# Optimization experiments

Measured on AMD Instinct MI355X. Metric: run time of the kernel, lower is better.

The kernel has to match this reference:

```python
import jax, jax.numpy as jnp
import numpy as np

H = 4096
N_HEADS = 32
N_KV = 8
HEAD_DIM = H // N_HEADS  # 128
GROUPS = N_HEADS // N_KV  # 4
FFN = 11008
EPS = 1e-5
B = 16
S_CACHE = 4096


def _rms(x, w):
    var = jnp.mean(x * x, axis=-1, keepdims=True)
    return w * (x * jax.lax.rsqrt(var + EPS))


def setup_inputs() -> dict:
    key = jax.random.key(0)
    ks = jax.random.split(key, 12)
    s = 0.02
    return {
        "hidden_states": jax.random.normal(ks[0], (B, 1, H), jnp.float32),
        "k_cache": jax.random.normal(ks[1], (B, N_KV, S_CACHE, HEAD_DIM), jnp.float32),
        "v_cache": jax.random.normal(ks[2], (B, N_KV, S_CACHE, HEAD_DIM), jnp.float32),
        "Wq": jax.random.normal(ks[3], (N_HEADS * HEAD_DIM, H), jnp.float32) * s,
        "Wk": jax.random.normal(ks[4], (N_KV * HEAD_DIM, H), jnp.float32) * s,
        "Wv": jax.random.normal(ks[5], (N_KV * HEAD_DIM, H), jnp.float32) * s,
        "Wo": jax.random.normal(ks[6], (H, N_HEADS * HEAD_DIM), jnp.float32) * s,
        "Wg": jax.random.normal(ks[7], (FFN, H), jnp.float32) * s,
        "Wu": jax.random.normal(ks[8], (FFN, H), jnp.float32) * s,
        "Wd": jax.random.normal(ks[9], (H, FFN), jnp.float32) * s,
        "ln1_w": jnp.ones((H,), jnp.float32),
        "ln2_w": jnp.ones((H,), jnp.float32),
    }


def reference(hidden_states, k_cache, v_cache, Wq, Wk, Wv, Wo, Wg, Wu, Wd, ln1_w, ln2_w):
    b = hidden_states.shape[0]
    residual = hidden_states
    h = _rms(hidden_states, ln1_w)  # [B,1,H]

    q = (h @ Wq.T).reshape(b, N_KV, GROUPS, HEAD_DIM)       # [B,kvH,G,D]
    k_new = (h @ Wk.T).reshape(b, N_KV, 1, HEAD_DIM)         # [B,kvH,1,D]
    v_new = (h @ Wv.T).reshape(b, N_KV, 1, HEAD_DIM)

    k = jnp.concatenate([k_cache, k_new], axis=2)            # [B,kvH,S+1,D]
    v = jnp.concatenate([v_cache, v_new], axis=2)

    scale = 1.0 / np.sqrt(HEAD_DIM)
    # GQA without materializing repeated KV heads (same math as repeat_interleave)
    scores = jnp.einsum("bkgd,bksd->bkgs", q, k) * scale      # [B,kvH,G,S+1]
    probs = jax.nn.softmax(scores.astype(jnp.float32), axis=-1).astype(q.dtype)
    attn = jnp.einsum("bkgs,bksd->bkgd", probs, v)            # [B,kvH,G,D]
    attn = attn.reshape(b, 1, N_HEADS * HEAD_DIM)

    h = residual + attn @ Wo.T                                # [B,1,H]

    residual = h
    h = _rms(h, ln2_w)
    mlp = (jax.nn.silu(h @ Wg.T) * (h @ Wu.T)) @ Wd.T
    return residual + mlp
```

## Files before the change

### kernel.cpp

```cpp
#include <hip/hip_runtime.h>
#include <math.h>

#define HH   4096
#define NKV  8
#define GRP  4
#define HD   128
#define FFN  11008
#define NB   16
#define SC   4096
#define SCALE 0.08838834764831845f
#define SCH  512

typedef float f4v __attribute__((ext_vector_type(4)));
typedef float f32x4 __attribute__((ext_vector_type(4)));
typedef short bf16x8 __attribute__((ext_vector_type(8)));
typedef unsigned short u16x4 __attribute__((ext_vector_type(4)));

__device__ __forceinline__ f4v ntload4(const float* p) {
  return __builtin_nontemporal_load((const f4v*)p);
}
__device__ __forceinline__ float dot4(f4v a, f4v b) {
  return a[0] * b[0] + a[1] * b[1] + a[2] * b[2] + a[3] * b[3];
}
__device__ __forceinline__ unsigned short f2bf(float f) {
  unsigned int u = __builtin_bit_cast(unsigned int, f);
  u += 0x7fffu + ((u >> 16) & 1u);
  return (unsigned short)(u >> 16);
}

__global__ void rmsnorm_bf_k(const float* __restrict__ x, const float* __restrict__ w,
                             unsigned short* __restrict__ y) {
  int b = blockIdx.x;
  const float* xb = x + (size_t)b * HH;
  unsigned short* yb = y + (size_t)b * HH;
  int t = threadIdx.x, lane = t & 63, wave = t >> 6;
  f4v v[4];
  float ss = 0.f;
#pragma unroll
  for (int i = 0; i < 4; ++i) {
    v[i] = *(const f4v*)(xb + 4 * (t + 256 * i));
    ss += dot4(v[i], v[i]);
  }
#pragma unroll
  for (int m = 1; m < 64; m <<= 1) ss += __shfl_xor(ss, m);
  __shared__ float red[4];
  if (lane == 0) red[wave] = ss;
  __syncthreads();
  float tot = red[0] + red[1] + red[2] + red[3];
  float rs = rsqrtf(tot * (1.0f / HH) + 1e-5f);
#pragma unroll
  for (int i = 0; i < 4; ++i) {
    int h = 4 * (t + 256 * i);
    f4v wv = *(const f4v*)(w + h);
    f4v o = v[i] * rs * wv;
    u16x4 p;
#pragma unroll
    for (int j = 0; j < 4; ++j) p[j] = f2bf(o[j]);
    *(u16x4*)(yb + h) = p;
  }
}

template <int MODE>
__global__ __launch_bounds__(256, 4) void gemv_mfma_k(
    const float* __restrict__ W0, const float* __restrict__ W1,
    const float* __restrict__ W2, const unsigned short* __restrict__ xbf,
    float* __restrict__ part, int O, int H, int CH) {
  int t = threadIdx.x, lane = t & 63, wave = t >> 6;
  int rb = blockIdx.x, kc = blockIdx.y;
  int obase = rb * 64 + wave * 16;
  int orow = obase + (lane & 15);

  const float* Wp;
  if (MODE == 0) {
    if (orow < 4096) Wp = W0 + (size_t)orow * H;
    else if (orow < 5120) Wp = W1 + (size_t)(orow - 4096) * H;
    else Wp = W2 + (size_t)(orow - 5120) * H;
  } else if (MODE == 2) {
    Wp = (orow < FFN) ? W0 + (size_t)orow * H : W1 + (size_t)(orow - FFN) * H;
  } else {
    Wp = W0 + (size_t)orow * H;
  }

  int k0 = kc * CH + (lane >> 4) * 8;
  const float* wp = Wp + k0;
  const unsigned short* ap = xbf + (size_t)(lane & 15) * H + k0;

  f32x4 acc = {0.f, 0.f, 0.f, 0.f};
  int steps = CH / 32;
#pragma unroll 2
  for (int s = 0; s < steps; ++s) {
    f4v w0 = ntload4(wp);
    f4v w1 = ntload4(wp + 4);
    bf16x8 a = *(const bf16x8*)ap;
    bf16x8 bb;
#pragma unroll
    for (int j = 0; j < 4; ++j) {
      bb[j] = (short)f2bf(w0[j]);
      bb[4 + j] = (short)f2bf(w1[j]);
    }
    acc = __builtin_amdgcn_mfma_f32_16x16x32_bf16(a, bb, acc, 0, 0, 0);
    wp += 32;
    ap += 32;
  }
  float* pb = part + ((size_t)kc * NB + (size_t)((lane >> 4) * 4)) * O + orow;
#pragma unroll
  for (int r = 0; r < 4; ++r) pb[(size_t)r * O] = acc[r];
}

__global__ void red_qkv_k(const float* __restrict__ pq, float* __restrict__ qb,
                          float* __restrict__ kn, float* __restrict__ vn) {
  int idx = blockIdx.x * 256 + threadIdx.x;
  int oi = idx % 1536, b = idx / 1536;
  int o = oi * 4;
  f4v s = {0.f, 0.f, 0.f, 0.f};
#pragma unroll
  for (int ks = 0; ks < 4; ++ks)
    s += *(const f4v*)(pq + ((size_t)(ks * NB + b)) * 6144 + o);
  if (o < 4096) *(f4v*)(qb + (size_t)b * 4096 + o) = s;
  else if (o < 5120) *(f4v*)(kn + (size_t)b * 1024 + (o - 4096)) = s;
  else *(f4v*)(vn + (size_t)b * 1024 + (o - 5120)) = s;
}

__global__ void rmsnorm2_k(const float* __restrict__ hid, const float* __restrict__ p1,
                           const float* __restrict__ w, float* __restrict__ h2,
                           unsigned short* __restrict__ xn2) {
  int b = blockIdx.x;
  int t = threadIdx.x, lane = t & 63, wave = t >> 6;
  f4v v[4];
  float ss = 0.f;
#pragma unroll
  for (int i = 0; i < 4; ++i) {
    int h = 4 * (t + 256 * i);
    f4v s = *(const f4v*)(hid + (size_t)b * HH + h);
#pragma unroll
    for (int ks = 0; ks < 8; ++ks)
      s += *(const f4v*)(p1 + ((size_t)(ks * NB + b)) * HH + h);
    v[i] = s;
    ss += dot4(s, s);
  }
#pragma unroll
  for (int m = 1; m < 64; m <<= 1) ss += __shfl_xor(ss, m);
  __shared__ float red[4];
  if (lane == 0) red[wave] = ss;
  __syncthreads();
  float tot = red[0] + red[1] + red[2] + red[3];
  float rs = rsqrtf(tot * (1.0f / HH) + 1e-5f);
#pragma unroll
  for (int i = 0; i < 4; ++i) {
    int h = 4 * (t + 256 * i);
    *(f4v*)(h2 + (size_t)b * HH + h) = v[i];
    f4v wv = *(const f4v*)(w + h);
    f4v o = v[i] * rs * wv;
    u16x4 p;
#pragma unroll
    for (int j = 0; j < 4; ++j) p[j] = f2bf(o[j]);
    *(u16x4*)(xn2 + (size_t)b * HH + h) = p;
  }
}

__global__ void red_gu_k(const float* __restrict__ p2, unsigned short* __restrict__ gu) {
  int idx = blockIdx.x * 256 + threadIdx.x;
  int pi = idx % 2752, b = idx / 2752;
  int p = pi * 4;
  const float* g0 = p2 + (size_t)b * 22016 + p;
  f4v g = *(const f4v*)g0 + *(const f4v*)(g0 + (size_t)NB * 22016);
  f4v u = *(const f4v*)(g0 + FFN) + *(const f4v*)(g0 + FFN + (size_t)NB * 22016);
  u16x4 pk;
#pragma unroll
  for (int j = 0; j < 4; ++j) {
    float gg = g[j];
    pk[j] = f2bf(gg / (1.f + __expf(-gg)) * u[j]);
  }
  *(u16x4*)(gu + (size_t)b * FFN + p) = pk;
}

__global__ void red_out_k(const float* __restrict__ h2, const float* __restrict__ p3,
                          float* __restrict__ out) {
  int idx = blockIdx.x * 256 + threadIdx.x;
  int o = (idx & 1023) * 4, b = idx >> 10;
  f4v s = *(const f4v*)(h2 + (size_t)b * HH + o);
#pragma unroll
  for (int ks = 0; ks < 8; ++ks)
    s += *(const f4v*)(p3 + ((size_t)(ks * NB + b)) * HH + o);
  *(f4v*)(out + (size_t)b * HH + o) = s;
}

__global__ __launch_bounds__(256, 4) void attn_part_k(
    const float* __restrict__ q, const float* __restrict__ kc,
    const float* __restrict__ vc, float* __restrict__ pm,
    float* __restrict__ pl, float* __restrict__ pacc) {
  int c = blockIdx.x, kv = blockIdx.y, b = blockIdx.z;
  int t = threadIdx.x, lane = t & 63, wave = t >> 6;
  int ds = lane & 15, ss = lane >> 4;
  __shared__ float sc[GRP][SCH];
  __shared__ float mg[GRP];
  __shared__ float accw[4][GRP][HD];
  __shared__ float lw[4][GRP];

  f4v qv[GRP][2];
  const float* qb = q + (size_t)b * HH + (size_t)kv * GRP * HD;
#pragma unroll
  for (int g = 0; g < GRP; ++g) {
    qv[g][0] = *(const f4v*)(qb + g * HD + 8 * ds);
    qv[g][1] = *(const f4v*)(qb + g * HD + 8 * ds + 4);
  }
  const size_t kvoff = ((size_t)b * NKV + kv) * (size_t)SC * HD;
  const float* kb = kc + kvoff;

  for (int st = 0; st < SCH / 16; ++st) {
    int sl = st * 16 + wave * 4 + ss;
    const float* kr = kb + (size_t)(c * SCH + sl) * HD + 8 * ds;
    f4v k0 = ntload4(kr);
    f4v k1 = ntload4(kr + 4);
    float d[GRP];
#pragma unroll
    for (int g = 0; g < GRP; ++g)
      d[g] = dot4(qv[g][0], k0) + dot4(qv[g][1], k1);
#pragma unroll
    for (int m = 1; m < 16; m <<= 1)
#pragma unroll
      for (int g = 0; g < GRP; ++g) d[g] += __shfl_xor(d[g], m);
    if (ds < GRP) sc[ds][sl] = d[ds] * SCALE;
  }
  __syncthreads();

  {
    int g = wave;
    float m = -1e30f;
    for (int i = lane; i < SCH; i += 64) m = fmaxf(m, sc[g][i]);
#pragma unroll
    for (int mm = 1; mm < 64; mm <<= 1) m = fmaxf(m, __shfl_xor(m, mm));
    if (lane == 0) mg[g] = m;
  }
  __syncthreads();
  float mreg[GRP];
#pragma unroll
  for (int g = 0; g < GRP; ++g) mreg[g] = mg[g];

  float acc[GRP][8];
  float lacc[GRP];
#pragma unroll
  for (int g = 0; g < GRP; ++g) {
    lacc[g] = 0.f;
#pragma unroll
    for (int j = 0; j < 8; ++j) acc[g][j] = 0.f;
  }
  const float* vb = vc + kvoff;
  for (int st = 0; st < SCH / 16; ++st) {
    int sl = st * 16 + wave * 4 + ss;
    const float* vr = vb + (size_t)(c * SCH + sl) * HD + 8 * ds;
    f4v v0 = ntload4(vr);
    f4v v1 = ntload4(vr + 4);
    float p[GRP];
#pragma unroll
    for (int g = 0; g < GRP; ++g) p[g] = __expf(sc[g][sl] - mreg[g]);
    if (ds == 0) {
#pragma unroll
      for (int g = 0; g < GRP; ++g) lacc[g] += p[g];
    }
#pragma unroll
    for (int g = 0; g < GRP; ++g) {
#pragma unroll
      for (int j = 0; j < 4; ++j) {
        acc[g][j] += p[g] * v0[j];
        acc[g][4 + j] += p[g] * v1[j];
      }
    }
  }
#pragma unroll
  for (int m = 16; m < 64; m <<= 1) {
#pragma unroll
    for (int g = 0; g < GRP; ++g) {
#pragma unroll
      for (int j = 0; j < 8; ++j) acc[g][j] += __shfl_xor(acc[g][j], m);
      lacc[g] += __shfl_xor(lacc[g], m);
    }
  }
  if (ss == 0) {
#pragma unroll
    for (int g = 0; g < GRP; ++g) {
#pragma unroll
      for (int j = 0; j < 4; ++j) {
        accw[wave][g][8 * ds + j] = acc[g][j];
        accw[wave][g][8 * ds + 4 + j] = acc[g][4 + j];
      }
    }
    if (ds == 0) {
#pragma unroll
      for (int g = 0; g < GRP; ++g) lw[wave][g] = lacc[g];
    }
  }
  __syncthreads();

  size_t pbase = (((size_t)(b * NKV + kv)) * 8 + c) * GRP;
  for (int idx = t; idx < GRP * HD; idx += 256) {
    int g = idx >> 7, dd = idx & 127;
    float o = accw[0][g][dd] + accw[1][g][dd] + accw[2][g][dd] + accw[3][g][dd];
    pacc[(pbase + g) * HD + dd] = o;
  }
  if (t < GRP) {
    pm[pbase + t] = mg[t];
    pl[pbase + t] = lw[0][t] + lw[1][t] + lw[2][t] + lw[3][t];
  }
}

__global__ void attn_red_k(const float* __restrict__ q, const float* __restrict__ knew,
                           const float* __restrict__ vnew, const float* __restrict__ pm,
                           const float* __restrict__ pl, const float* __restrict__ pacc,
                           unsigned short* __restrict__ attnb) {
  int bi = blockIdx.x;
  int b = bi >> 3, kv = bi & 7;
  int t = threadIdx.x, lane = t & 63, wave = t >> 6;
  __shared__ float sn[GRP];
  {
    int g = wave;
    float2 qv = *(const float2*)(q + (size_t)b * HH + (size_t)(kv * GRP + g) * HD + 2 * lane);
    float2 k2 = *(const float2*)(knew + (size_t)b * (NKV * HD) + kv * HD + 2 * lane);
    float d = qv.x * k2.x + qv.y * k2.y;
#pragma unroll
    for (int m = 1; m < 64; m <<= 1) d += __shfl_xor(d, m);
    if (lane == 0) sn[g] = d * SCALE;
  }
  __syncthreads();
  size_t base = ((size_t)(b * NKV + kv)) * 8;
  for (int idx = t; idx < GRP * HD; idx += 256) {
    int g = idx >> 7, dd = idx & 127;
    float snv = sn[g];
    float M = snv;
    float pmv[8];
#pragma unroll
    for (int cc = 0; cc < 8; ++cc) {
      pmv[cc] = pm[(base + cc) * GRP + g];
      M = fmaxf(M, pmv[cc]);
    }
    float en = __expf(snv - M);
    float L = en;
    float o = en * vnew[(size_t)b * (NKV * HD) + kv * HD + dd];
#pragma unroll
    for (int cc = 0; cc < 8; ++cc) {
      float f = __expf(pmv[cc] - M);
      L += f * pl[(base + cc) * GRP + g];
      o += f * pacc[((base + cc) * GRP + g) * HD + dd];
    }
    attnb[(size_t)b * HH + (size_t)(kv * GRP + g) * HD + dd] = f2bf(o / L);
  }
}

extern "C" void kernel_launch(void* const* d_in, const int* in_sizes, int n_in,
                              void* d_out, int out_size, void* d_ws, size_t ws_size,
                              hipStream_t stream) {
  const float* hidden = (const float*)d_in[0];
  const float* kc = (const float*)d_in[1];
  const float* vc = (const float*)d_in[2];
  const float* Wq = (const float*)d_in[3];
  const float* Wk = (const float*)d_in[4];
  const float* Wv = (const float*)d_in[5];
  const float* Wo = (const float*)d_in[6];
  const float* Wg = (const float*)d_in[7];
  const float* Wu = (const float*)d_in[8];
  const float* Wd = (const float*)d_in[9];
  const float* ln1 = (const float*)d_in[10];
  const float* ln2 = (const float*)d_in[11];
  float* out = (float*)d_out;

  float* ws = (float*)d_ws;
  float* p = ws;
  unsigned short* xn1bf = (unsigned short*)p;  p += 32768;
  float* qb = p;    p += 65536;
  float* kn = p;    p += 16384;
  float* vn = p;    p += 16384;
  unsigned short* attnbf = (unsigned short*)p; p += 32768;
  float* h2 = p;    p += 65536;
  unsigned short* xn2bf = (unsigned short*)p;  p += 32768;
  unsigned short* gubf = (unsigned short*)p;   p += 88064;
  float* pm = p;    p += 4096;
  float* pl = p;    p += 4096;
  float* pacc = p;  p += 524288;
  float* pq = p;    p += 393216;
  float* p1 = p;    p += 524288;
  float* p2 = p;    p += 704512;
  float* p3 = p;    p += 524288;

  rmsnorm_bf_k<<<16, 256, 0, stream>>>(hidden, ln1, xn1bf);
  gemv_mfma_k<0><<<dim3(96, 4), 256, 0, stream>>>(Wq, Wk, Wv, xn1bf, pq, 6144, 4096, 1024);
  red_qkv_k<<<96, 256, 0, stream>>>(pq, qb, kn, vn);
  attn_part_k<<<dim3(8, 8, 16), 256, 0, stream>>>(qb, kc, vc, pm, pl, pacc);
  attn_red_k<<<128, 256, 0, stream>>>(qb, kn, vn, pm, pl, pacc, attnbf);
  gemv_mfma_k<1><<<dim3(64, 8), 256, 0, stream>>>(Wo, nullptr, nullptr, attnbf, p1, 4096, 4096, 512);
  rmsnorm2_k<<<16, 256, 0, stream>>>(hidden, p1, ln2, h2, xn2bf);
  gemv_mfma_k<2><<<dim3(344, 2), 256, 0, stream>>>(Wg, Wu, nullptr, xn2bf, p2, 22016, 4096, 2048);
  red_gu_k<<<172, 256, 0, stream>>>(p2, gubf);
  gemv_mfma_k<3><<<dim3(64, 8), 256, 0, stream>>>(Wd, nullptr, nullptr, gubf, p3, 4096, 11008, 1376);
  red_out_k<<<64, 256, 0, stream>>>(h2, p3, out);
}
```

Measured before the change: 286.3 us.

## Fuse QKV split-K reduction into attention kernels and use MFMA for QK scores

Removes the separate red_qkv_k launch by summing the split-K partials for q, k_new and v_new directly inside attn_part_k and attn_red_k. The QK score pass now converts K and q to bf16 and computes the dot products with 16x16x32 MFMA instructions instead of scalar dot products plus shuffles. The exp and row-sum are done once in the softmax pass and stored in shared memory, so the V pass only reads the probabilities. This removes a launch and cuts ALU work in the score pass, but it lowers QK precision to bf16 and drops the nontemporal hint on K loads. Workspace buffer sizes are also shrunk.

```diff
diff --git a/kernel.cpp b/kernel.cpp
--- a/kernel.cpp
+++ b/kernel.cpp
@@ -15,6 +15,7 @@
 typedef float f32x4 __attribute__((ext_vector_type(4)));
 typedef short bf16x8 __attribute__((ext_vector_type(8)));
 typedef unsigned short u16x4 __attribute__((ext_vector_type(4)));
+typedef unsigned int u32x4v __attribute__((ext_vector_type(4)));
 
 __device__ __forceinline__ f4v ntload4(const float* p) {
   return __builtin_nontemporal_load((const f4v*)p);
@@ -26,6 +27,12 @@
   unsigned int u = __builtin_bit_cast(unsigned int, f);
   u += 0x7fffu + ((u >> 16) & 1u);
   return (unsigned short)(u >> 16);
+}
+__device__ __forceinline__ float silu_f(float g) { return g / (1.f + __expf(-g)); }
+__device__ __forceinline__ unsigned int cvtpk(float lo, float hi) {
+  unsigned int r;
+  asm("v_cvt_pk_bf16_f32 %0, %1, %2" : "=v"(r) : "v"(lo), "v"(hi));
+  return r;
 }
 
 __global__ void rmsnorm_bf_k(const float* __restrict__ x, const float* __restrict__ w,
@@ -107,20 +114,6 @@
   for (int r = 0; r < 4; ++r) pb[(size_t)r * O] = acc[r];
 }
 
-__global__ void red_qkv_k(const float* __restrict__ pq, float* __restrict__ qb,
-                          float* __restrict__ kn, float* __restrict__ vn) {
-  int idx = blockIdx.x * 256 + threadIdx.x;
-  int oi = idx % 1536, b = idx / 1536;
-  int o = oi * 4;
-  f4v s = {0.f, 0.f, 0.f, 0.f};
-#pragma unroll
-  for (int ks = 0; ks < 4; ++ks)
-    s += *(const f4v*)(pq + ((size_t)(ks * NB + b)) * 6144 + o);
-  if (o < 4096) *(f4v*)(qb + (size_t)b * 4096 + o) = s;
-  else if (o < 5120) *(f4v*)(kn + (size_t)b * 1024 + (o - 4096)) = s;
-  else *(f4v*)(vn + (size_t)b * 1024 + (o - 5120)) = s;
-}
-
 __global__ void rmsnorm2_k(const float* __restrict__ hid, const float* __restrict__ p1,
                            const float* __restrict__ w, float* __restrict__ h2,
                            unsigned short* __restrict__ xn2) {
@@ -167,10 +160,7 @@
   f4v u = *(const f4v*)(g0 + FFN) + *(const f4v*)(g0 + FFN + (size_t)NB * 22016);
   u16x4 pk;
 #pragma unroll
-  for (int j = 0; j < 4; ++j) {
-    float gg = g[j];
-    pk[j] = f2bf(gg / (1.f + __expf(-gg)) * u[j]);
-  }
+  for (int j = 0; j < 4; ++j) pk[j] = f2bf(silu_f(g[j]) * u[j]);
   *(u16x4*)(gu + (size_t)b * FFN + p) = pk;
 }
 
@@ -186,66 +176,98 @@
 }
 
 __global__ __launch_bounds__(256, 4) void attn_part_k(
-    const float* __restrict__ q, const float* __restrict__ kc,
-    const float* __restrict__ vc, float* __restrict__ pm,
+    const float* __restrict__ pq, const float* __restrict__ kcache,
+    const float* __restrict__ vcache, float* __restrict__ pm,
     float* __restrict__ pl, float* __restrict__ pacc) {
   int c = blockIdx.x, kv = blockIdx.y, b = blockIdx.z;
   int t = threadIdx.x, lane = t & 63, wave = t >> 6;
   int ds = lane & 15, ss = lane >> 4;
+  __shared__ float qs[GRP * HD];
   __shared__ float sc[GRP][SCH];
-  __shared__ float mg[GRP];
   __shared__ float accw[4][GRP][HD];
-  __shared__ float lw[4][GRP];
-
-  f4v qv[GRP][2];
-  const float* qb = q + (size_t)b * HH + (size_t)kv * GRP * HD;
-#pragma unroll
-  for (int g = 0; g < GRP; ++g) {
-    qv[g][0] = *(const f4v*)(qb + g * HD + 8 * ds);
-    qv[g][1] = *(const f4v*)(qb + g * HD + 8 * ds + 4);
-  }
+
+  {
+    int i0 = t * 2;
+#pragma unroll
+    for (int i = i0; i < i0 + 2; ++i) {
+      int off = kv * (GRP * HD) + i;
+      float s = 0.f;
+#pragma unroll
+      for (int kk = 0; kk < 4; ++kk)
+        s += pq[((size_t)kk * NB + b) * 6144 + off];
+      qs[i] = s;
+    }
+  }
+  __syncthreads();
+
+  bf16x8 bq[4];
+#pragma unroll
+  for (int kk = 0; kk < 4; ++kk) {
+    u32x4v w;
+#pragma unroll
+    for (int jj = 0; jj < 4; ++jj) {
+      float f0 = 0.f, f1 = 0.f;
+      if (ds < GRP) {
+        int d = kk * 32 + ss * 8 + jj * 2;
+        f0 = qs[ds * HD + d];
+        f1 = qs[ds * HD + d + 1];
+      }
+      w[jj] = cvtpk(f0, f1);
+    }
+    bq[kk] = __builtin_bit_cast(bf16x8, w);
+  }
+
   const size_t kvoff = ((size_t)b * NKV + kv) * (size_t)SC * HD;
-  const float* kb = kc + kvoff;
-
-  for (int st = 0; st < SCH / 16; ++st) {
-    int sl = st * 16 + wave * 4 + ss;
-    const float* kr = kb + (size_t)(c * SCH + sl) * HD + 8 * ds;
-    f4v k0 = ntload4(kr);
-    f4v k1 = ntload4(kr + 4);
-    float d[GRP];
-#pragma unroll
-    for (int g = 0; g < GRP; ++g)
-      d[g] = dot4(qv[g][0], k0) + dot4(qv[g][1], k1);
-#pragma unroll
-    for (int m = 1; m < 16; m <<= 1)
-#pragma unroll
-      for (int g = 0; g < GRP; ++g) d[g] += __shfl_xor(d[g], m);
-    if (ds < GRP) sc[ds][sl] = d[ds] * SCALE;
-  }
-  __syncthreads();
-
+  const float* kb = kcache + kvoff;
+
+  for (int st = 0; st < SCH / 64; ++st) {
+    int prel = (st * 4 + wave) * 16;
+    const float* kr = kb + (size_t)(c * SCH + prel + ds) * HD + ss * 8;
+    f32x4 d4 = {0.f, 0.f, 0.f, 0.f};
+#pragma unroll
+    for (int kk = 0; kk < 4; ++kk) {
+      f4v k0 = *(const f4v*)(kr + kk * 32);
+      f4v k1 = *(const f4v*)(kr + kk * 32 + 4);
+      u32x4v w;
+      w[0] = cvtpk(k0[0], k0[1]);
+      w[1] = cvtpk(k0[2], k0[3]);
+      w[2] = cvtpk(k1[0], k1[1]);
+      w[3] = cvtpk(k1[2], k1[3]);
+      d4 = __builtin_amdgcn_mfma_f32_16x16x32_bf16(
+          __builtin_bit_cast(bf16x8, w), bq[kk], d4, 0, 0, 0);
+    }
+    if (ds < GRP) {
+#pragma unroll
+      for (int r = 0; r < 4; ++r) sc[ds][prel + ss * 4 + r] = d4[r] * SCALE;
+    }
+  }
+  __syncthreads();
+
+  size_t pbase = (((size_t)(b * NKV + kv)) * 8 + c) * GRP;
   {
     int g = wave;
     float m = -1e30f;
     for (int i = lane; i < SCH; i += 64) m = fmaxf(m, sc[g][i]);
 #pragma unroll
     for (int mm = 1; mm < 64; mm <<= 1) m = fmaxf(m, __shfl_xor(m, mm));
-    if (lane == 0) mg[g] = m;
-  }
-  __syncthreads();
-  float mreg[GRP];
-#pragma unroll
-  for (int g = 0; g < GRP; ++g) mreg[g] = mg[g];
+    float lsum = 0.f;
+    for (int i = lane; i < SCH; i += 64) {
+      float e = __expf(sc[g][i] - m);
+      sc[g][i] = e;
+      lsum += e;
+    }
+#pragma unroll
+    for (int mm = 1; mm < 64; mm <<= 1) lsum += __shfl_xor(lsum, mm);
+    if (lane == 0) { pm[pbase + g] = m; pl[pbase + g] = lsum; }
+  }
+  __syncthreads();
 
   float acc[GRP][8];
-  float lacc[GRP];
-#pragma unroll
-  for (int g = 0; g < GRP; ++g) {
-    lacc[g] = 0.f;
+#pragma unroll
+  for (int g = 0; g < GRP; ++g)
 #pragma unroll
     for (int j = 0; j < 8; ++j) acc[g][j] = 0.f;
-  }
-  const float* vb = vc + kvoff;
+  const float* vb = vcache + kvoff;
   for (int st = 0; st < SCH / 16; ++st) {
     int sl = st * 16 + wave * 4 + ss;
     const float* vr = vb + (size_t)(c * SCH + sl) * HD + 8 * ds;
@@ -253,11 +275,7 @@
     f4v v1 = ntload4(vr + 4);
     float p[GRP];
 #pragma unroll
-    for (int g = 0; g < GRP; ++g) p[g] = __expf(sc[g][sl] - mreg[g]);
-    if (ds == 0) {
-#pragma unroll
-      for (int g = 0; g < GRP; ++g) lacc[g] += p[g];
-    }
+    for (int g = 0; g < GRP; ++g) p[g] = sc[g][sl];
 #pragma unroll
     for (int g = 0; g < GRP; ++g) {
 #pragma unroll
@@ -268,44 +286,30 @@
     }
   }
 #pragma unroll
-  for (int m = 16; m < 64; m <<= 1) {
-#pragma unroll
-    for (int g = 0; g < GRP; ++g) {
+  for (int m = 16; m < 64; m <<= 1)
+#pragma unroll
+    for (int g = 0; g < GRP; ++g)
 #pragma unroll
       for (int j = 0; j < 8; ++j) acc[g][j] += __shfl_xor(acc[g][j], m);
-      lacc[g] += __shfl_xor(lacc[g], m);
-    }
-  }
   if (ss == 0) {
 #pragma unroll
-    for (int g = 0; g < GRP; ++g) {
+    for (int g = 0; g < GRP; ++g)
 #pragma unroll
       for (int j = 0; j < 4; ++j) {
         accw[wave][g][8 * ds + j] = acc[g][j];
         accw[wave][g][8 * ds + 4 + j] = acc[g][4 + j];
       }
-    }
-    if (ds == 0) {
-#pragma unroll
-      for (int g = 0; g < GRP; ++g) lw[wave][g] = lacc[g];
-    }
-  }
-  __syncthreads();
-
-  size_t pbase = (((size_t)(b * NKV + kv)) * 8 + c) * GRP;
+  }
+  __syncthreads();
+
   for (int idx = t; idx < GRP * HD; idx += 256) {
     int g = idx >> 7, dd = idx & 127;
     float o = accw[0][g][dd] + accw[1][g][dd] + accw[2][g][dd] + accw[3][g][dd];
     pacc[(pbase + g) * HD + dd] = o;
   }
-  if (t < GRP) {
-    pm[pbase + t] = mg[t];
-    pl[pbase + t] = lw[0][t] + lw[1][t] + lw[2][t] + lw[3][t];
-  }
-}
-
-__global__ void attn_red_k(const float* __restrict__ q, const float* __restrict__ knew,
-                           const float* __restrict__ vnew, const float* __restrict__ pm,
+}
+
+__global__ void attn_red_k(const float* __restrict__ pq, const float* __restrict__ pm,
                            const float* __restrict__ pl, const float* __restrict__ pacc,
                            unsigned short* __restrict__ attnb) {
   int bi = blockIdx.x;
@@ -314,9 +318,16 @@
   __shared__ float sn[GRP];
   {
     int g = wave;
-    float2 qv = *(const float2*)(q + (size_t)b * HH + (size_t)(kv * GRP + g) * HD + 2 * lane);
-    float2 k2 = *(const float2*)(knew + (size_t)b * (NKV * HD) + kv * HD + 2 * lane);
-    float d = qv.x * k2.x + qv.y * k2.y;
+    int qoff = kv * (GRP * HD) + g * HD + 2 * lane;
+    int koff = 4096 + kv * HD + 2 * lane;
+    float qx = 0.f, qy = 0.f, kx = 0.f, ky = 0.f;
+#pragma unroll
+    for (int kk = 0; kk < 4; ++kk) {
+      const float* pp = pq + ((size_t)kk * NB + b) * 6144;
+      qx += pp[qoff]; qy += pp[qoff + 1];
+      kx += pp[koff]; ky += pp[koff + 1];
+    }
+    float d = qx * kx + qy * ky;
 #pragma unroll
     for (int m = 1; m < 64; m <<= 1) d += __shfl_xor(d, m);
     if (lane == 0) sn[g] = d * SCALE;
@@ -333,9 +344,13 @@
       pmv[cc] = pm[(base + cc) * GRP + g];
       M = fmaxf(M, pmv[cc]);
     }
+    float vnv = 0.f;
+#pragma unroll
+    for (int kk = 0; kk < 4; ++kk)
+      vnv += pq[((size_t)kk * NB + b) * 6144 + 5120 + kv * HD + dd];
     float en = __expf(snv - M);
     float L = en;
-    float o = en * vnew[(size_t)b * (NKV * HD) + kv * HD + dd];
+    float o = en * vnv;
 #pragma unroll
     for (int cc = 0; cc < 8; ++cc) {
       float f = __expf(pmv[cc] - M);
@@ -363,15 +378,11 @@
   const float* ln2 = (const float*)d_in[11];
   float* out = (float*)d_out;
 
-  float* ws = (float*)d_ws;
-  float* p = ws;
-  unsigned short* xn1bf = (unsigned short*)p;  p += 32768;
-  float* qb = p;    p += 65536;
-  float* kn = p;    p += 16384;
-  float* vn = p;    p += 16384;
-  unsigned short* attnbf = (unsigned short*)p; p += 32768;
+  float* p = (float*)d_ws;
+  unsigned short* xn1bf = (unsigned short*)p;  p += 16384;
+  unsigned short* attnbf = (unsigned short*)p; p += 16384;
   float* h2 = p;    p += 65536;
-  unsigned short* xn2bf = (unsigned short*)p;  p += 32768;
+  unsigned short* xn2bf = (unsigned short*)p;  p += 16384;
   unsigned short* gubf = (unsigned short*)p;   p += 88064;
   float* pm = p;    p += 4096;
   float* pl = p;    p += 4096;
@@ -383,9 +394,8 @@
 
   rmsnorm_bf_k<<<16, 256, 0, stream>>>(hidden, ln1, xn1bf);
   gemv_mfma_k<0><<<dim3(96, 4), 256, 0, stream>>>(Wq, Wk, Wv, xn1bf, pq, 6144, 4096, 1024);
-  red_qkv_k<<<96, 256, 0, stream>>>(pq, qb, kn, vn);
-  attn_part_k<<<dim3(8, 8, 16), 256, 0, stream>>>(qb, kc, vc, pm, pl, pacc);
-  attn_red_k<<<128, 256, 0, stream>>>(qb, kn, vn, pm, pl, pacc, attnbf);
+  attn_part_k<<<dim3(8, 8, 16), 256, 0, stream>>>(pq, kc, vc, pm, pl, pacc);
+  attn_red_k<<<128, 256, 0, stream>>>(pq, pm, pl, pacc, attnbf);
   gemv_mfma_k<1><<<dim3(64, 8), 256, 0, stream>>>(Wo, nullptr, nullptr, attnbf, p1, 4096, 4096, 512);
   rmsnorm2_k<<<16, 256, 0, stream>>>(hidden, p1, ln2, h2, xn2bf);
   gemv_mfma_k<2><<<dim3(344, 2), 256, 0, stream>>>(Wg, Wu, nullptr, xn2bf, p2, 22016, 4096, 2048);
```

New measurement: 286.8 us. No clear change (+0.2%).
